# Performance work log

Hardware: AMD Instinct MI355X
Metric: run time of the kernel (lower is better)

Reference implementation:

```python
import jax, jax.numpy as jnp
import numpy as np

N_NODES = 50000
N_EDGES = 1_250_000
D_FEAT = 64


def setup_inputs() -> dict:
    key = jax.random.key(0)
    k1, k2, k3 = jax.random.split(key, 3)
    graph_embedding = jax.random.normal(k1, (N_NODES, D_FEAT), dtype=jnp.float32)
    src = jax.random.randint(k2, (N_EDGES,), 0, N_NODES, dtype=jnp.int64)
    dst = jax.random.randint(k3, (N_EDGES,), 0, N_NODES, dtype=jnp.int64)
    return {"graph_embedding": graph_embedding, "src": src, "dst": dst}


def reference(graph_embedding, src, dst):
    # DGL update_all(copy_u('ft','m'), sum('m','ft')):
    # out[v] = sum over edges (u->v) of graph_embedding[u]
    messages = graph_embedding[src]  # [E, d] gather
    out = jax.ops.segment_sum(messages, dst, num_segments=graph_embedding.shape[0])
    return out
```

## Files before the change

kernel.cpp:

```cpp
#include <hip/hip_runtime.h>


#define D_FEAT 64
#define NB2    512
#define CAPB   3072
#define MAXNB  512
#define PCHUNK 8192
#define CAP1   96

static __device__ __forceinline__ unsigned short f2bf(float f) {
    unsigned u = __float_as_uint(f);
    u += 0x7fffu + ((u >> 16) & 1u);
    return (unsigned short)(u >> 16);
}

__global__ __launch_bounds__(512) void fused_cvt_partition_kernel(
    const float4* __restrict__ emb4,
    uint2*        __restrict__ embh2,
    const int*    __restrict__ src,
    const int*    __restrict__ dst,
    unsigned*     __restrict__ cursor,
    unsigned*     __restrict__ packed,
    int n4, int cvt_blocks, int n_edges, unsigned npb_inv)
{
    __shared__ unsigned lpk[PCHUNK];
    __shared__ unsigned lhist[MAXNB];
    __shared__ unsigned lbase[MAXNB];

    if ((int)blockIdx.x < cvt_blocks) {
        int i = blockIdx.x * 512 + threadIdx.x;
        if (i < n4) {
            float4 x = emb4[i];
            uint2 o;
            o.x = (unsigned)f2bf(x.x) | ((unsigned)f2bf(x.y) << 16);
            o.y = (unsigned)f2bf(x.z) | ((unsigned)f2bf(x.w) << 16);
            embh2[i] = o;
        }
        return;
    }

    int pb   = blockIdx.x - cvt_blocks;
    int t    = threadIdx.x;
    int base = pb * PCHUNK;
    int cnt  = n_edges - base; if (cnt > PCHUNK) cnt = PCHUNK; if (cnt < 0) cnt = 0;

    for (int i = t; i < MAXNB; i += 512) lhist[i] = 0;
    __syncthreads();

    int nv = cnt >> 2;
    const int4* d4 = (const int4*)(dst + base);
    const int4* s4 = (const int4*)(src + base);
    for (int i = t; i < nv; i += 512) {
        int4 d = d4[i];
        int4 s = s4[i];
        uint4 pkw;
        pkw.x = ((unsigned)d.x << 16) | (unsigned)s.x;
        pkw.y = ((unsigned)d.y << 16) | (unsigned)s.y;
        pkw.z = ((unsigned)d.z << 16) | (unsigned)s.z;
        pkw.w = ((unsigned)d.w << 16) | (unsigned)s.w;
        ((uint4*)lpk)[i] = pkw;
        atomicAdd(&lhist[__umulhi(pkw.x >> 16, npb_inv)], 1u);
        atomicAdd(&lhist[__umulhi(pkw.y >> 16, npb_inv)], 1u);
        atomicAdd(&lhist[__umulhi(pkw.z >> 16, npb_inv)], 1u);
        atomicAdd(&lhist[__umulhi(pkw.w >> 16, npb_inv)], 1u);
    }
    for (int i = nv * 4 + t; i < cnt; i += 512) {
        unsigned dd = (unsigned)dst[base + i];
        lpk[i] = (dd << 16) | (unsigned)src[base + i];
        atomicAdd(&lhist[__umulhi(dd, npb_inv)], 1u);
    }
    __syncthreads();

    for (int i = t; i < MAXNB; i += 512) {
        unsigned c = lhist[i];
        lbase[i] = c ? atomicAdd(&cursor[i], c) : 0u;
        lhist[i] = 0;
    }
    __syncthreads();

    for (int i = t; i < cnt; i += 512) {
        unsigned p = lpk[i];
        unsigned b = __umulhi(p >> 16, npb_inv);
        unsigned off = atomicAdd(&lhist[b], 1u);
        unsigned pos = lbase[b] + off;
        if (pos < CAPB)
            packed[(size_t)b * CAPB + pos] = p;
    }
}

#define ACC8(h, q0,q1,q2,q3,q4,q5,q6,q7) \
    q0 += __uint_as_float(h.x << 16);           \
    q1 += __uint_as_float(h.x & 0xffff0000u);   \
    q2 += __uint_as_float(h.y << 16);           \
    q3 += __uint_as_float(h.y & 0xffff0000u);   \
    q4 += __uint_as_float(h.z << 16);           \
    q5 += __uint_as_float(h.z & 0xffff0000u);   \
    q6 += __uint_as_float(h.w << 16);           \
    q7 += __uint_as_float(h.w & 0xffff0000u);

__global__ __launch_bounds__(1024) void sortgather_kernel(
    const unsigned short* __restrict__ embh,
    const unsigned*       __restrict__ cursor,
    const unsigned*       __restrict__ packed,
    float*                __restrict__ out,
    int n_nodes, unsigned npb)
{
    __shared__ unsigned       lpk[CAPB];
    __shared__ unsigned short slist[CAPB];
    __shared__ unsigned       hist[128];
    __shared__ unsigned       cur[128];
    __shared__ unsigned       stc[128];

    int b = blockIdx.x;
    int t = threadIdx.x;
    int node_base = (int)(b * npb);
    int nn = n_nodes - node_base;
    if (nn > (int)npb) nn = (int)npb;
    if (nn < 0) nn = 0;

    int cnt = (int)cursor[b]; if (cnt > CAPB) cnt = CAPB;
    const unsigned* pk = packed + (size_t)b * CAPB;

    if (t < 128) hist[t] = 0;
    __syncthreads();

    for (int i = t; i < cnt; i += 1024) {
        unsigned p = pk[i];
        lpk[i] = p;
        atomicAdd(&hist[(p >> 16) - node_base], 1u);
    }
    __syncthreads();

    if (t < 64) {
        int l = t;
        unsigned v0 = hist[2 * l], v1 = hist[2 * l + 1];
        unsigned s = v0 + v1;
        unsigned inc = s;
        #pragma unroll
        for (int d = 1; d < 64; d <<= 1) {
            unsigned u = __shfl_up(inc, d);
            if (l >= d) inc += u;
        }
        unsigned exc = inc - s;
        cur[2 * l]     = exc;
        cur[2 * l + 1] = exc + v0;
        stc[2 * l]     = (exc << 16) | v0;
        stc[2 * l + 1] = ((exc + v0) << 16) | v1;
    }
    __syncthreads();

    for (int i = t; i < cnt; i += 1024) {
        unsigned p = lpk[i];
        unsigned pos = atomicAdd(&cur[(p >> 16) - node_base], 1u);
        slist[pos] = (unsigned short)(p & 0xffffu);
    }
    __syncthreads();

    int w    = t >> 6;
    int lane = t & 63;
    int rgrp = lane >> 3;
    int c8   = lane & 7;

    for (int dlA = w; dlA < 128; dlA += 32) {
        int dlB = dlA + 16;
        unsigned scA = stc[dlA];
        unsigned scB = stc[dlB];
        int stA = (int)(scA >> 16), cnA = (int)(scA & 0xffffu);
        int stB = (int)(scB >> 16), cnB = (int)(scB & 0xffffu);

        float a0=0.f,a1=0.f,a2=0.f,a3=0.f,a4=0.f,a5=0.f,a6=0.f,a7=0.f;
        float b0=0.f,b1=0.f,b2=0.f,b3=0.f,b4=0.f,b5=0.f,b6=0.f,b7=0.f;
        int mx = cnA > cnB ? cnA : cnB;
        for (int j = 0; j < mx; j += 16) {
            int r0 = j + rgrp;
            int r1 = j + 8 + rgrp;
            bool vA0 = r0 < cnA, vA1 = r1 < cnA;
            bool vB0 = r0 < cnB, vB1 = r1 < cnB;
            uint4 hA0, hA1, hB0, hB1;
            if (vA0) hA0 = *(const uint4*)(embh + ((size_t)slist[stA + r0] << 6) + c8 * 8);
            if (vA1) hA1 = *(const uint4*)(embh + ((size_t)slist[stA + r1] << 6) + c8 * 8);
            if (vB0) hB0 = *(const uint4*)(embh + ((size_t)slist[stB + r0] << 6) + c8 * 8);
            if (vB1) hB1 = *(const uint4*)(embh + ((size_t)slist[stB + r1] << 6) + c8 * 8);
            if (vA0) { ACC8(hA0, a0,a1,a2,a3,a4,a5,a6,a7); }
            if (vA1) { ACC8(hA1, a0,a1,a2,a3,a4,a5,a6,a7); }
            if (vB0) { ACC8(hB0, b0,b1,b2,b3,b4,b5,b6,b7); }
            if (vB1) { ACC8(hB1, b0,b1,b2,b3,b4,b5,b6,b7); }
        }
        #define RED16(mask) \
            a0 += __shfl_xor(a0, mask); a1 += __shfl_xor(a1, mask); \
            a2 += __shfl_xor(a2, mask); a3 += __shfl_xor(a3, mask); \
            a4 += __shfl_xor(a4, mask); a5 += __shfl_xor(a5, mask); \
            a6 += __shfl_xor(a6, mask); a7 += __shfl_xor(a7, mask); \
            b0 += __shfl_xor(b0, mask); b1 += __shfl_xor(b1, mask); \
            b2 += __shfl_xor(b2, mask); b3 += __shfl_xor(b3, mask); \
            b4 += __shfl_xor(b4, mask); b5 += __shfl_xor(b5, mask); \
            b6 += __shfl_xor(b6, mask); b7 += __shfl_xor(b7, mask);
        RED16(8); RED16(16); RED16(32);
        #undef RED16

        if (lane < 8 && dlA < nn) {
            float4* o4 = (float4*)(out + (size_t)(node_base + dlA) * D_FEAT + lane * 8);
            o4[0] = make_float4(a0, a1, a2, a3);
            o4[1] = make_float4(a4, a5, a6, a7);
        }
        if (lane < 8 && dlB < nn) {
            float4* o4 = (float4*)(out + (size_t)(node_base + dlB) * D_FEAT + lane * 8);
            o4[0] = make_float4(b0, b1, b2, b3);
            o4[1] = make_float4(b4, b5, b6, b7);
        }
    }
}

__global__ __launch_bounds__(256) void count_scatter_kernel(
    const int* __restrict__ src, const int* __restrict__ dst,
    int* __restrict__ cnt, int* __restrict__ bucket, int n_edges)
{
    int e = blockIdx.x * blockDim.x + threadIdx.x;
    if (e >= n_edges) return;
    int s = src[e], d = dst[e];
    int pos = atomicAdd(&cnt[d], 1);
    if (pos < CAP1) bucket[(size_t)d * CAP1 + pos] = s;
}

__global__ __launch_bounds__(256) void gather_sum_kernel(
    const float* __restrict__ emb, const int* __restrict__ cnt,
    const int* __restrict__ bucket, float* __restrict__ out, int n_nodes)
{
    int v = (blockIdx.x * blockDim.x + threadIdx.x) >> 6;
    int lane = threadIdx.x & 63;
    if (v >= n_nodes) return;
    int n = cnt[v]; if (n > CAP1) n = CAP1;
    const int* b = bucket + (size_t)v * CAP1;
    float acc = 0.f;
    for (int j = 0; j < n; ++j)
        acc += emb[(size_t)b[j] * D_FEAT + lane];
    out[(size_t)v * D_FEAT + lane] = acc;
}

__global__ __launch_bounds__(256) void scatter_sum_fallback(
    const float* __restrict__ emb, const int* __restrict__ src,
    const int* __restrict__ dst, float* __restrict__ out, int n_edges)
{
    int gid = blockIdx.x * blockDim.x + threadIdx.x;
    int e = gid >> 4;
    if (e >= n_edges) return;
    int c = gid & 15;
    int s = src[e], d = dst[e];
    const float4* emb4 = (const float4*)emb;
    float4 v = emb4[(size_t)s * 16 + c];
    float* o = out + (size_t)d * D_FEAT + c * 4;
    atomicAdd(o + 0, v.x); atomicAdd(o + 1, v.y);
    atomicAdd(o + 2, v.z); atomicAdd(o + 3, v.w);
}

extern "C" void kernel_launch(void* const* d_in, const int* in_sizes, int n_in,
                              void* d_out, int out_size, void* d_ws, size_t ws_size,
                              hipStream_t stream) {
    const float* emb = (const float*)d_in[0];
    const int*   src = (const int*)d_in[1];
    const int*   dst = (const int*)d_in[2];
    float*       out = (float*)d_out;

    int n_edges = in_sizes[1];
    int n_nodes = out_size / D_FEAT;

    unsigned npb = (unsigned)((n_nodes + NB2 - 1) / NB2);
    if (npb == 0) npb = 1;
    int nb = (n_nodes + (int)npb - 1) / (int)npb;
    unsigned npb_inv = (unsigned)((0x100000000ULL + npb - 1) / npb);

    size_t cur_b  = 4096;
    size_t pack_b = (size_t)MAXNB * CAPB * sizeof(unsigned);
    size_t embh_b = (size_t)n_nodes * D_FEAT * sizeof(unsigned short);

    if (n_nodes <= 65536 && npb <= 128 && nb <= MAXNB &&
        ws_size >= cur_b + pack_b + embh_b) {
        char* p = (char*)d_ws;
        unsigned*       cursor = (unsigned*)p;        p += cur_b;
        unsigned*       packed = (unsigned*)p;        p += pack_b;
        unsigned short* embh   = (unsigned short*)p;

        hipMemsetAsync(cursor, 0, (size_t)MAXNB * sizeof(unsigned), stream);

        int n4 = n_nodes * D_FEAT / 4;
        int cvt_blocks = (n4 + 511) / 512;
        int p_blocks   = (n_edges + PCHUNK - 1) / PCHUNK;
        fused_cvt_partition_kernel<<<cvt_blocks + p_blocks, 512, 0, stream>>>(
            (const float4*)emb, (uint2*)embh, src, dst, cursor, packed,
            n4, cvt_blocks, n_edges, npb_inv);

        sortgather_kernel<<<nb, 1024, 0, stream>>>(
            embh, cursor, packed, out, n_nodes, npb);
    } else if (ws_size >= (size_t)n_nodes * sizeof(int) * (1 + CAP1)) {
        int* cnt    = (int*)d_ws;
        int* bucket = (int*)((char*)d_ws + (size_t)n_nodes * sizeof(int));
        hipMemsetAsync(cnt, 0, (size_t)n_nodes * sizeof(int), stream);
        count_scatter_kernel<<<(n_edges + 255) / 256, 256, 0, stream>>>(
            src, dst, cnt, bucket, n_edges);
        gather_sum_kernel<<<(n_nodes * 64 + 255) / 256, 256, 0, stream>>>(
            emb, cnt, bucket, out, n_nodes);
    } else {
        hipMemsetAsync(d_out, 0, (size_t)out_size * sizeof(float), stream);
        long long total = (long long)n_edges * 16;
        scatter_sum_fallback<<<(int)((total + 255) / 256), 256, 0, stream>>>(
            emb, src, dst, out, n_edges);
    }
}
```

Before: 113.9 us.

## Split bf16 embedding table into two column halves and gather per half

The conversion kernel now writes the bf16 embedding as two separate tables, one per 32-column half. The gather phase runs two passes, one per half, and each row fetch is 64 bytes instead of 128. The goal is to halve the working set of each pass so the random gathers hit more often in L2/MALL. In exchange the slot lists are re-read twice, reductions take an extra shuffle step, and a block barrier is added between passes. Loads of the packed edge list and stores to the output also become nontemporal hints.

```diff
diff --git a/kernel.cpp b/kernel.cpp
--- a/kernel.cpp
+++ b/kernel.cpp
@@ -7,6 +7,8 @@
 #define MAXNB  512
 #define PCHUNK 8192
 #define CAP1   96
+
+typedef float f4v __attribute__((ext_vector_type(4)));
 
 static __device__ __forceinline__ unsigned short f2bf(float f) {
     unsigned u = __float_as_uint(f);
@@ -34,7 +36,10 @@
             uint2 o;
             o.x = (unsigned)f2bf(x.x) | ((unsigned)f2bf(x.y) << 16);
             o.y = (unsigned)f2bf(x.z) | ((unsigned)f2bf(x.w) << 16);
-            embh2[i] = o;
+            int n = i >> 4;
+            int q = i & 15;
+            uint2* tb = embh2 + ((q & 8) ? (n4 >> 1) : 0);
+            tb[n * 8 + (q & 7)] = o;
         }
         return;
     }
@@ -125,7 +130,7 @@
     __syncthreads();
 
     for (int i = t; i < cnt; i += 1024) {
-        unsigned p = pk[i];
+        unsigned p = __builtin_nontemporal_load(pk + i);
         lpk[i] = p;
         atomicAdd(&hist[(p >> 16) - node_base], 1u);
     }
@@ -158,56 +163,66 @@
 
     int w    = t >> 6;
     int lane = t & 63;
-    int rgrp = lane >> 3;
-    int c8   = lane & 7;
-
-    for (int dlA = w; dlA < 128; dlA += 32) {
-        int dlB = dlA + 16;
-        unsigned scA = stc[dlA];
-        unsigned scB = stc[dlB];
-        int stA = (int)(scA >> 16), cnA = (int)(scA & 0xffffu);
-        int stB = (int)(scB >> 16), cnB = (int)(scB & 0xffffu);
-
-        float a0=0.f,a1=0.f,a2=0.f,a3=0.f,a4=0.f,a5=0.f,a6=0.f,a7=0.f;
-        float b0=0.f,b1=0.f,b2=0.f,b3=0.f,b4=0.f,b5=0.f,b6=0.f,b7=0.f;
-        int mx = cnA > cnB ? cnA : cnB;
-        for (int j = 0; j < mx; j += 16) {
-            int r0 = j + rgrp;
-            int r1 = j + 8 + rgrp;
-            bool vA0 = r0 < cnA, vA1 = r1 < cnA;
-            bool vB0 = r0 < cnB, vB1 = r1 < cnB;
-            uint4 hA0, hA1, hB0, hB1;
-            if (vA0) hA0 = *(const uint4*)(embh + ((size_t)slist[stA + r0] << 6) + c8 * 8);
-            if (vA1) hA1 = *(const uint4*)(embh + ((size_t)slist[stA + r1] << 6) + c8 * 8);
-            if (vB0) hB0 = *(const uint4*)(embh + ((size_t)slist[stB + r0] << 6) + c8 * 8);
-            if (vB1) hB1 = *(const uint4*)(embh + ((size_t)slist[stB + r1] << 6) + c8 * 8);
-            if (vA0) { ACC8(hA0, a0,a1,a2,a3,a4,a5,a6,a7); }
-            if (vA1) { ACC8(hA1, a0,a1,a2,a3,a4,a5,a6,a7); }
-            if (vB0) { ACC8(hB0, b0,b1,b2,b3,b4,b5,b6,b7); }
-            if (vB1) { ACC8(hB1, b0,b1,b2,b3,b4,b5,b6,b7); }
+    int rgrp = lane >> 2;
+    int c4   = lane & 3;
+    size_t halfoff = (size_t)n_nodes << 5;
+
+    for (int ph = 0; ph < 2; ++ph) {
+        const unsigned short* tb = embh + (size_t)ph * halfoff;
+
+        for (int dlA = w; dlA < 128; dlA += 32) {
+            int dlB = dlA + 16;
+            unsigned scA = stc[dlA];
+            unsigned scB = stc[dlB];
+            int stA = (int)(scA >> 16), cnA = (int)(scA & 0xffffu);
+            int stB = (int)(scB >> 16), cnB = (int)(scB & 0xffffu);
+
+            float a0=0.f,a1=0.f,a2=0.f,a3=0.f,a4=0.f,a5=0.f,a6=0.f,a7=0.f;
+            float b0=0.f,b1=0.f,b2=0.f,b3=0.f,b4=0.f,b5=0.f,b6=0.f,b7=0.f;
+            int mx = cnA > cnB ? cnA : cnB;
+            for (int j = 0; j < mx; j += 32) {
+                int r0 = j + rgrp;
+                int r1 = j + 16 + rgrp;
+                bool vA0 = r0 < cnA, vA1 = r1 < cnA;
+                bool vB0 = r0 < cnB, vB1 = r1 < cnB;
+                uint4 hA0, hA1, hB0, hB1;
+                if (vA0) hA0 = *(const uint4*)(tb + ((size_t)slist[stA + r0] << 5) + c4 * 8);
+                if (vA1) hA1 = *(const uint4*)(tb + ((size_t)slist[stA + r1] << 5) + c4 * 8);
+                if (vB0) hB0 = *(const uint4*)(tb + ((size_t)slist[stB + r0] << 5) + c4 * 8);
+                if (vB1) hB1 = *(const uint4*)(tb + ((size_t)slist[stB + r1] << 5) + c4 * 8);
+                if (vA0) { ACC8(hA0, a0,a1,a2,a3,a4,a5,a6,a7); }
+                if (vA1) { ACC8(hA1, a0,a1,a2,a3,a4,a5,a6,a7); }
+                if (vB0) { ACC8(hB0, b0,b1,b2,b3,b4,b5,b6,b7); }
+                if (vB1) { ACC8(hB1, b0,b1,b2,b3,b4,b5,b6,b7); }
+            }
+            #define RED16(mask) \
+                a0 += __shfl_xor(a0, mask); a1 += __shfl_xor(a1, mask); \
+                a2 += __shfl_xor(a2, mask); a3 += __shfl_xor(a3, mask); \
+                a4 += __shfl_xor(a4, mask); a5 += __shfl_xor(a5, mask); \
+                a6 += __shfl_xor(a6, mask); a7 += __shfl_xor(a7, mask); \
+                b0 += __shfl_xor(b0, mask); b1 += __shfl_xor(b1, mask); \
+                b2 += __shfl_xor(b2, mask); b3 += __shfl_xor(b3, mask); \
+                b4 += __shfl_xor(b4, mask); b5 += __shfl_xor(b5, mask); \
+                b6 += __shfl_xor(b6, mask); b7 += __shfl_xor(b7, mask);
+            RED16(4); RED16(8); RED16(16); RED16(32);
+            #undef RED16
+
+            if (lane < 4 && dlA < nn) {
+                float* o = out + (size_t)(node_base + dlA) * D_FEAT + ph * 32 + lane * 8;
+                f4v v0 = {a0, a1, a2, a3};
+                f4v v1 = {a4, a5, a6, a7};
+                __builtin_nontemporal_store(v0, (f4v*)o);
+                __builtin_nontemporal_store(v1, (f4v*)(o + 4));
+            }
+            if (lane < 4 && dlB < nn) {
+                float* o = out + (size_t)(node_base + dlB) * D_FEAT + ph * 32 + lane * 8;
+                f4v v0 = {b0, b1, b2, b3};
+                f4v v1 = {b4, b5, b6, b7};
+                __builtin_nontemporal_store(v0, (f4v*)o);
+                __builtin_nontemporal_store(v1, (f4v*)(o + 4));
+            }
         }
-        #define RED16(mask) \
-            a0 += __shfl_xor(a0, mask); a1 += __shfl_xor(a1, mask); \
-            a2 += __shfl_xor(a2, mask); a3 += __shfl_xor(a3, mask); \
-            a4 += __shfl_xor(a4, mask); a5 += __shfl_xor(a5, mask); \
-            a6 += __shfl_xor(a6, mask); a7 += __shfl_xor(a7, mask); \
-            b0 += __shfl_xor(b0, mask); b1 += __shfl_xor(b1, mask); \
-            b2 += __shfl_xor(b2, mask); b3 += __shfl_xor(b3, mask); \
-            b4 += __shfl_xor(b4, mask); b5 += __shfl_xor(b5, mask); \
-            b6 += __shfl_xor(b6, mask); b7 += __shfl_xor(b7, mask);
-        RED16(8); RED16(16); RED16(32);
-        #undef RED16
-
-        if (lane < 8 && dlA < nn) {
-            float4* o4 = (float4*)(out + (size_t)(node_base + dlA) * D_FEAT + lane * 8);
-            o4[0] = make_float4(a0, a1, a2, a3);
-            o4[1] = make_float4(a4, a5, a6, a7);
-        }
-        if (lane < 8 && dlB < nn) {
-            float4* o4 = (float4*)(out + (size_t)(node_base + dlB) * D_FEAT + lane * 8);
-            o4[0] = make_float4(b0, b1, b2, b3);
-            o4[1] = make_float4(b4, b5, b6, b7);
-        }
+        __syncthreads();
     }
 }
 
```

Result: slower. 146.2 us (+28.4%).

## Assign one 8-lane group per destination node in sortgather, drop shuffle reduction

Applied to the files above, without the earlier changes.

Changes the gather-sum work mapping: instead of each wavefront handling two nodes with 8 row groups and a cross-lane shuffle reduction, each group of 8 threads now owns one node and serially accumulates up to 8 neighbor rows per iteration. This removes the shuffle reduction and the padding waste of pairing nodes, and adds a minimum-waves hint to launch bounds. In exchange, load balance depends on per-node degree within a wavefront (the loop runs to the max degree among 8 nodes), and there is less memory-level parallelism per node.

```diff
diff --git a/kernel.cpp b/kernel.cpp
--- a/kernel.cpp
+++ b/kernel.cpp
@@ -88,17 +88,17 @@
     }
 }
 
-#define ACC8(h, q0,q1,q2,q3,q4,q5,q6,q7) \
-    q0 += __uint_as_float(h.x << 16);           \
-    q1 += __uint_as_float(h.x & 0xffff0000u);   \
-    q2 += __uint_as_float(h.y << 16);           \
-    q3 += __uint_as_float(h.y & 0xffff0000u);   \
-    q4 += __uint_as_float(h.z << 16);           \
-    q5 += __uint_as_float(h.z & 0xffff0000u);   \
-    q6 += __uint_as_float(h.w << 16);           \
-    q7 += __uint_as_float(h.w & 0xffff0000u);
-
-__global__ __launch_bounds__(1024) void sortgather_kernel(
+#define ACC8(h) \
+    a0 += __uint_as_float(h.x << 16);           \
+    a1 += __uint_as_float(h.x & 0xffff0000u);   \
+    a2 += __uint_as_float(h.y << 16);           \
+    a3 += __uint_as_float(h.y & 0xffff0000u);   \
+    a4 += __uint_as_float(h.z << 16);           \
+    a5 += __uint_as_float(h.z & 0xffff0000u);   \
+    a6 += __uint_as_float(h.w << 16);           \
+    a7 += __uint_as_float(h.w & 0xffff0000u);
+
+__global__ __launch_bounds__(1024, 8) void sortgather_kernel(
     const unsigned short* __restrict__ embh,
     const unsigned*       __restrict__ cursor,
     const unsigned*       __restrict__ packed,
@@ -156,58 +156,40 @@
     }
     __syncthreads();
 
-    int w    = t >> 6;
-    int lane = t & 63;
-    int rgrp = lane >> 3;
-    int c8   = lane & 7;
-
-    for (int dlA = w; dlA < 128; dlA += 32) {
-        int dlB = dlA + 16;
-        unsigned scA = stc[dlA];
-        unsigned scB = stc[dlB];
-        int stA = (int)(scA >> 16), cnA = (int)(scA & 0xffffu);
-        int stB = (int)(scB >> 16), cnB = (int)(scB & 0xffffu);
-
-        float a0=0.f,a1=0.f,a2=0.f,a3=0.f,a4=0.f,a5=0.f,a6=0.f,a7=0.f;
-        float b0=0.f,b1=0.f,b2=0.f,b3=0.f,b4=0.f,b5=0.f,b6=0.f,b7=0.f;
-        int mx = cnA > cnB ? cnA : cnB;
-        for (int j = 0; j < mx; j += 16) {
-            int r0 = j + rgrp;
-            int r1 = j + 8 + rgrp;
-            bool vA0 = r0 < cnA, vA1 = r1 < cnA;
-            bool vB0 = r0 < cnB, vB1 = r1 < cnB;
-            uint4 hA0, hA1, hB0, hB1;
-            if (vA0) hA0 = *(const uint4*)(embh + ((size_t)slist[stA + r0] << 6) + c8 * 8);
-            if (vA1) hA1 = *(const uint4*)(embh + ((size_t)slist[stA + r1] << 6) + c8 * 8);
-            if (vB0) hB0 = *(const uint4*)(embh + ((size_t)slist[stB + r0] << 6) + c8 * 8);
-            if (vB1) hB1 = *(const uint4*)(embh + ((size_t)slist[stB + r1] << 6) + c8 * 8);
-            if (vA0) { ACC8(hA0, a0,a1,a2,a3,a4,a5,a6,a7); }
-            if (vA1) { ACC8(hA1, a0,a1,a2,a3,a4,a5,a6,a7); }
-            if (vB0) { ACC8(hB0, b0,b1,b2,b3,b4,b5,b6,b7); }
-            if (vB1) { ACC8(hB1, b0,b1,b2,b3,b4,b5,b6,b7); }
-        }
-        #define RED16(mask) \
-            a0 += __shfl_xor(a0, mask); a1 += __shfl_xor(a1, mask); \
-            a2 += __shfl_xor(a2, mask); a3 += __shfl_xor(a3, mask); \
-            a4 += __shfl_xor(a4, mask); a5 += __shfl_xor(a5, mask); \
-            a6 += __shfl_xor(a6, mask); a7 += __shfl_xor(a7, mask); \
-            b0 += __shfl_xor(b0, mask); b1 += __shfl_xor(b1, mask); \
-            b2 += __shfl_xor(b2, mask); b3 += __shfl_xor(b3, mask); \
-            b4 += __shfl_xor(b4, mask); b5 += __shfl_xor(b5, mask); \
-            b6 += __shfl_xor(b6, mask); b7 += __shfl_xor(b7, mask);
-        RED16(8); RED16(16); RED16(32);
-        #undef RED16
-
-        if (lane < 8 && dlA < nn) {
-            float4* o4 = (float4*)(out + (size_t)(node_base + dlA) * D_FEAT + lane * 8);
-            o4[0] = make_float4(a0, a1, a2, a3);
-            o4[1] = make_float4(a4, a5, a6, a7);
-        }
-        if (lane < 8 && dlB < nn) {
-            float4* o4 = (float4*)(out + (size_t)(node_base + dlB) * D_FEAT + lane * 8);
-            o4[0] = make_float4(b0, b1, b2, b3);
-            o4[1] = make_float4(b4, b5, b6, b7);
-        }
+    int g  = t >> 3;
+    int l8 = t & 7;
+
+    unsigned sc = stc[g];
+    int st = (int)(sc >> 16), cn = (int)(sc & 0xffffu);
+
+    float a0=0.f,a1=0.f,a2=0.f,a3=0.f,a4=0.f,a5=0.f,a6=0.f,a7=0.f;
+
+    for (int j = 0; j < cn; j += 8) {
+        bool v1 = j + 1 < cn, v2 = j + 2 < cn, v3 = j + 3 < cn;
+        bool v4 = j + 4 < cn, v5 = j + 5 < cn, v6 = j + 6 < cn, v7 = j + 7 < cn;
+        uint4 h0, h1, h2, h3, h4, h5, h6, h7;
+        h0 =          *(const uint4*)(embh + ((size_t)slist[st + j    ] << 6) + l8 * 8);
+        if (v1) h1 =  *(const uint4*)(embh + ((size_t)slist[st + j + 1] << 6) + l8 * 8);
+        if (v2) h2 =  *(const uint4*)(embh + ((size_t)slist[st + j + 2] << 6) + l8 * 8);
+        if (v3) h3 =  *(const uint4*)(embh + ((size_t)slist[st + j + 3] << 6) + l8 * 8);
+        if (v4) h4 =  *(const uint4*)(embh + ((size_t)slist[st + j + 4] << 6) + l8 * 8);
+        if (v5) h5 =  *(const uint4*)(embh + ((size_t)slist[st + j + 5] << 6) + l8 * 8);
+        if (v6) h6 =  *(const uint4*)(embh + ((size_t)slist[st + j + 6] << 6) + l8 * 8);
+        if (v7) h7 =  *(const uint4*)(embh + ((size_t)slist[st + j + 7] << 6) + l8 * 8);
+        { ACC8(h0); }
+        if (v1) { ACC8(h1); }
+        if (v2) { ACC8(h2); }
+        if (v3) { ACC8(h3); }
+        if (v4) { ACC8(h4); }
+        if (v5) { ACC8(h5); }
+        if (v6) { ACC8(h6); }
+        if (v7) { ACC8(h7); }
+    }
+
+    if (g < nn) {
+        float4* o4 = (float4*)(out + (size_t)(node_base + g) * D_FEAT + l8 * 8);
+        o4[0] = make_float4(a0, a1, a2, a3);
+        o4[1] = make_float4(a4, a5, a6, a7);
     }
 }
 
```

New measurement: 104.9 us. 1.09x faster.
